# Kernel optimization log

Measured on AMD Instinct MI355X. Metric: run time of the kernel, lower is better.

Reference implementation:

```python
import jax, jax.numpy as jnp
import numpy as np

N_NODES = 50000
N_EDGES = 800000
IN_DIM = 128
HIDDEN = 64
NEG_SLOPE = 0.2


def setup_inputs() -> dict:
    key = jax.random.key(0)
    ks = jax.random.split(key, 8)
    x = jax.random.normal(ks[0], (N_NODES, IN_DIM), dtype=jnp.float32)
    edge_index = jax.random.randint(ks[1], (2, N_EDGES), 0, N_NODES, dtype=jnp.int64)
    # GATConv params (heads=1)
    W = jax.random.normal(ks[2], (HIDDEN, IN_DIM), dtype=jnp.float32) / np.sqrt(IN_DIM)
    att_src = jax.random.normal(ks[3], (HIDDEN,), dtype=jnp.float32) / np.sqrt(HIDDEN)
    att_dst = jax.random.normal(ks[4], (HIDDEN,), dtype=jnp.float32) / np.sqrt(HIDDEN)
    bias_conv = jnp.zeros((HIDDEN,), dtype=jnp.float32)
    # final Linear(hidden, 1)
    W_lin = jax.random.normal(ks[5], (1, HIDDEN), dtype=jnp.float32) / np.sqrt(HIDDEN)
    b_lin = jnp.zeros((1,), dtype=jnp.float32)
    return {"x": x, "edge_index": edge_index, "W": W, "att_src": att_src,
            "att_dst": att_dst, "bias_conv": bias_conv, "W_lin": W_lin, "b_lin": b_lin}


def _gat_forward(x, edge_index, W, att_src, att_dst, bias_conv, W_lin, b_lin):
    n = x.shape[0]
    # add self-loops (PyG GATConv default)
    loop = jnp.arange(n, dtype=edge_index.dtype)
    src = jnp.concatenate([edge_index[0], loop])  # source nodes j (messages from)
    dst = jnp.concatenate([edge_index[1], loop])  # destination nodes i (aggregated at)

    h = x @ W.T                                   # [N, H] projected features
    a_src = h @ att_src                           # [N]
    a_dst = h @ att_dst                           # [N]

    e = jax.nn.leaky_relu(a_src[src] + a_dst[dst], NEG_SLOPE)  # [E']
    # segment softmax over incoming edges of each destination node
    m = jax.ops.segment_max(e, dst, num_segments=n)            # [N]
    ex = jnp.exp(e - m[dst])
    s = jax.ops.segment_sum(ex, dst, num_segments=n)           # [N]
    alpha = ex / s[dst]                                        # [E']

    out = jax.ops.segment_sum(alpha[:, None] * h[src], dst, num_segments=n)
    out = out + bias_conv                         # [N, H]

    out = jax.nn.relu(out)
    # dropout p=0.5 is a no-op in eval mode
    y = jax.nn.sigmoid(out @ W_lin.T + b_lin)     # [N, 1]
    return y


def reference(x, edge_index, W, att_src, att_dst, bias_conv, W_lin, b_lin):
    return _gat_forward(x, edge_index, W, att_src, att_dst, bias_conv, W_lin, b_lin)
```

## Files before the change

### kernel.cpp

```cpp
#include <hip/hip_runtime.h>
#include <hip/hip_bf16.h>
#include <hip/hip_fp16.h>
#include <cstdint>

#define IND 128
#define HID 64
#define NEG_SLOPE 0.2f
#define EPB 4096
#define CBSHIFT 8
#define BCAP 8192
#define SORT_THREADS 256
#define EPT (EPB / SORT_THREADS)
#define QCAP 2048
#define GT 512
#define GSCAN (BCAP / GT)

typedef __attribute__((ext_vector_type(8))) short bf16x8;
typedef __attribute__((ext_vector_type(4))) float f32x4;

__device__ __forceinline__ unsigned short f2bf_bits(float f) {
  __hip_bfloat16 b = __float2bfloat16(f);
  return *reinterpret_cast<unsigned short*>(&b);
}
__device__ __forceinline__ unsigned short f2h_bits(float f) {
  __half h = __float2half(f);
  return *reinterpret_cast<unsigned short*>(&h);
}
__device__ __forceinline__ float h2f_bits(unsigned short u) {
  __half_raw r; r.x = u;
  return __half2float(__half(r));
}
__device__ __forceinline__ float bf2f_bits(unsigned short u) {
  return __uint_as_float((unsigned)u << 16);
}
__device__ __forceinline__ unsigned pack_bf2(float lo, float hi) {
  return (unsigned)f2bf_bits(lo) | ((unsigned)f2bf_bits(hi) << 16);
}
__device__ __forceinline__ bf16x8 mk_bf16x8(unsigned a, unsigned b,
                                            unsigned c, unsigned d) {
  union { unsigned u[4]; bf16x8 v; } t;
  t.u[0] = a; t.u[1] = b; t.u[2] = c; t.u[3] = d;
  return t.v;
}
__device__ __forceinline__ bf16x8 mk_bf16x8_u4(uint4 u) {
  union { uint4 u4; bf16x8 v; } t;
  t.u4 = u;
  return t.v;
}

__global__ __launch_bounds__(256) void k_proj_sort(
    const float* __restrict__ x, const float* __restrict__ W,
    const float* __restrict__ att_s, const float* __restrict__ att_d,
    unsigned short* __restrict__ h, float* __restrict__ a_src,
    float* __restrict__ a_dst,
    const int* __restrict__ ei, int* __restrict__ gcur,
    unsigned* __restrict__ tmp, int E, long long E2,
    int nSort, int nbuck, int n)
{
  __shared__ __align__(16) char smem[20480];
  const int tid = threadIdx.x;

  if (blockIdx.x < (unsigned)nSort) {
    int* hist       = (int*)smem;
    int* sums       = hist + 256;
    int* cur        = sums + 256;
    int* gbase      = cur + 256;
    unsigned* sorted = (unsigned*)(gbase + 256);

    hist[tid] = 0;
    __syncthreads();

    const long long i0 = (long long)blockIdx.x * EPB;

    unsigned pk[EPT];
#pragma unroll
    for (int j = 0; j < EPT; ++j) {
      long long idx = i0 + j * SORT_THREADS + tid;
      unsigned v = 0xFFFFFFFFu;
      if (idx < E2) {
        int s, d;
        if (idx < E) { s = ei[idx]; d = ei[E + idx]; }
        else         { s = d = (int)(idx - E); }
        v = ((unsigned)d << 16) | (unsigned)s;
        atomicAdd(&hist[d >> CBSHIFT], 1);
      }
      pk[j] = v;
    }
    __syncthreads();

    sums[tid] = hist[tid];
    __syncthreads();
    for (int off = 1; off < 256; off <<= 1) {
      int t = (tid >= off) ? sums[tid - off] : 0;
      __syncthreads();
      sums[tid] += t;
      __syncthreads();
    }
    {
      const int lstart_t = sums[tid] - hist[tid];
      cur[tid] = lstart_t;
      gbase[tid] = (tid < nbuck && hist[tid] > 0)
                     ? tid * BCAP + atomicAdd(&gcur[tid], hist[tid]) : 0;
    }
    __syncthreads();
    hist[tid] = sums[tid] - hist[tid];
    __syncthreads();

#pragma unroll
    for (int j = 0; j < EPT; ++j) {
      unsigned v = pk[j];
      if (v != 0xFFFFFFFFu) {
        int b = v >> (16 + CBSHIFT);
        int lpos = atomicAdd(&cur[b], 1);
        sorted[lpos] = v;
      }
    }
    __syncthreads();

    const int cntE = (int)((E2 - i0 < EPB) ? (E2 - i0) : EPB);
    for (int i = tid; i < cntE; i += SORT_THREADS) {
      unsigned v = sorted[i];
      int b = v >> (16 + CBSHIFT);
      tmp[gbase[b] + (i - hist[b])] = v;
    }
    return;
  }

  unsigned* wt = (unsigned*)smem;

  const int nodeBase = (blockIdx.x - nSort) * 64;

#pragma unroll
  for (int it = 0; it < 4; ++it) {
    int fi = (it * 256 + tid) * 8;
    int row = fi >> 7, k = fi & 127;
    float4 w0 = *(const float4*)(W + fi);
    float4 w1 = *(const float4*)(W + fi + 4);
    uint4 pv;
    pv.x = pack_bf2(w0.x, w0.y);
    pv.y = pack_bf2(w0.z, w0.w);
    pv.z = pack_bf2(w1.x, w1.y);
    pv.w = pack_bf2(w1.z, w1.w);
    int c = (k >> 3) ^ ((row >> 2) & 7);
    ((uint4*)wt)[row * 16 + c] = pv;
  }
  __syncthreads();

  const int lane = tid & 63;
  const int wid4 = tid >> 6;
  const int r16  = lane & 15;
  const int q    = lane >> 4;

  const int arow = nodeBase + 16 * wid4 + r16;
  const size_t xoff = (size_t)((arow < n) ? arow : (n - 1)) * IND;

  float4 xv[8];
#pragma unroll
  for (int ks = 0; ks < 4; ++ks) {
    xv[2 * ks]     = *(const float4*)(x + xoff + 32 * ks + 8 * q);
    xv[2 * ks + 1] = *(const float4*)(x + xoff + 32 * ks + 8 * q + 4);
  }

  f32x4 acc0 = {0.f, 0.f, 0.f, 0.f};
  f32x4 acc1 = {0.f, 0.f, 0.f, 0.f};
  f32x4 acc2 = {0.f, 0.f, 0.f, 0.f};
  f32x4 acc3 = {0.f, 0.f, 0.f, 0.f};

#pragma unroll
  for (int ks = 0; ks < 4; ++ks) {
    float4 xa = xv[2 * ks], xb = xv[2 * ks + 1];
    bf16x8 afrag = mk_bf16x8(pack_bf2(xa.x, xa.y), pack_bf2(xa.z, xa.w),
                             pack_bf2(xb.x, xb.y), pack_bf2(xb.z, xb.w));
    {
      int row = r16;
      uint4 bw = ((const uint4*)wt)[row * 16 + ((4 * ks + q) ^ ((row >> 2) & 7))];
      acc0 = __builtin_amdgcn_mfma_f32_16x16x32_bf16(afrag, mk_bf16x8_u4(bw), acc0, 0, 0, 0);
    }
    {
      int row = 16 + r16;
      uint4 bw = ((const uint4*)wt)[row * 16 + ((4 * ks + q) ^ ((row >> 2) & 7))];
      acc1 = __builtin_amdgcn_mfma_f32_16x16x32_bf16(afrag, mk_bf16x8_u4(bw), acc1, 0, 0, 0);
    }
    {
      int row = 32 + r16;
      uint4 bw = ((const uint4*)wt)[row * 16 + ((4 * ks + q) ^ ((row >> 2) & 7))];
      acc2 = __builtin_amdgcn_mfma_f32_16x16x32_bf16(afrag, mk_bf16x8_u4(bw), acc2, 0, 0, 0);
    }
    {
      int row = 48 + r16;
      uint4 bw = ((const uint4*)wt)[row * 16 + ((4 * ks + q) ^ ((row >> 2) & 7))];
      acc3 = __builtin_amdgcn_mfma_f32_16x16x32_bf16(afrag, mk_bf16x8_u4(bw), acc3, 0, 0, 0);
    }
  }

  const float as0 = att_s[r16],      ad0 = att_d[r16];
  const float as1 = att_s[16 + r16], ad1 = att_d[16 + r16];
  const float as2 = att_s[32 + r16], ad2 = att_d[32 + r16];
  const float as3 = att_s[48 + r16], ad3 = att_d[48 + r16];

#pragma unroll
  for (int reg = 0; reg < 4; ++reg) {
    const int node = nodeBase + 16 * wid4 + 4 * q + reg;
    const bool ok = (node < n);
    if (ok) {
      const size_t hb = (size_t)node * HID;
      h[hb + r16]      = f2bf_bits(acc0[reg]);
      h[hb + 16 + r16] = f2bf_bits(acc1[reg]);
      h[hb + 32 + r16] = f2bf_bits(acc2[reg]);
      h[hb + 48 + r16] = f2bf_bits(acc3[reg]);
    }
    float ps = acc0[reg] * as0 + acc1[reg] * as1 + acc2[reg] * as2 + acc3[reg] * as3;
    float pd = acc0[reg] * ad0 + acc1[reg] * ad1 + acc2[reg] * ad2 + acc3[reg] * ad3;
    ps += __shfl_xor(ps, 1, 64); ps += __shfl_xor(ps, 2, 64);
    ps += __shfl_xor(ps, 4, 64); ps += __shfl_xor(ps, 8, 64);
    pd += __shfl_xor(pd, 1, 64); pd += __shfl_xor(pd, 2, 64);
    pd += __shfl_xor(pd, 4, 64); pd += __shfl_xor(pd, 8, 64);
    if (ok && r16 == 0) { a_src[node] = ps; a_dst[node] = pd; }
  }
}

__global__ __launch_bounds__(GT) void k_csr_gather(
    const unsigned* __restrict__ tmp, const int* __restrict__ gcur,
    const float* __restrict__ a_src, const float* __restrict__ a_dst,
    const unsigned short* __restrict__ h,
    const float* __restrict__ bias, const float* __restrict__ W_lin,
    const float* __restrict__ b_lin, float* __restrict__ y, int n)
{
  __shared__ int degl[64], sums[64], cur[64];
  __shared__ float adl[64];
  __shared__ unsigned csrw[QCAP];

  const int tid  = threadIdx.x;
  const int blk  = blockIdx.x;
  const int b    = blk >> 2;
  const int n0   = (b << CBSHIFT) + ((blk & 3) << 6);
  const int base = b * BCAP;
  const int next = base + gcur[b];

  if (tid < 64) {
    degl[tid] = 0;
    const int node = n0 + tid;
    adl[tid] = (node < n) ? a_dst[node] : 0.f;
  }
  __syncthreads();

  unsigned pkv[GSCAN];
#pragma unroll
  for (int j = 0; j < GSCAN; ++j) {
    int i = base + j * GT + tid;
    unsigned v = 0xFFFFFFFFu;
    if (i < next) {
      v = tmp[i];
      unsigned dl = (v >> 16) - (unsigned)n0;
      if (dl < 64u) atomicAdd(&degl[dl], 1);
      else v = 0xFFFFFFFFu;
    }
    pkv[j] = v;
  }
  __syncthreads();

  if (tid < 64) sums[tid] = degl[tid];
  __syncthreads();
  for (int off = 1; off < 64; off <<= 1) {
    int t = (tid >= off && tid < 64) ? sums[tid - off] : 0;
    __syncthreads();
    if (tid < 64) sums[tid] += t;
    __syncthreads();
  }
  if (tid < 64) cur[tid] = sums[tid] - degl[tid];
  __syncthreads();

#pragma unroll
  for (int j = 0; j < GSCAN; ++j) {
    unsigned v = pkv[j];
    if (v != 0xFFFFFFFFu) {
      unsigned dl = (v >> 16) - (unsigned)n0;
      int s = (int)(v & 0xFFFFu);
      float sc = a_src[s] + adl[dl];
      sc = (sc >= 0.f) ? sc : NEG_SLOPE * sc;
      float w = expf(sc);
      int pos = atomicAdd(&cur[dl], 1);
      if (pos < QCAP)
        csrw[pos] = (unsigned)s | ((unsigned)f2h_bits(w) << 16);
    }
  }
  __syncthreads();

  const int lane    = tid & 63;
  const int wid     = tid >> 6;
  const int quarter = lane >> 4;
  const int sub     = lane & 15;

  for (int nl = wid; nl < 64; nl += 8) {
    const int node = n0 + nl;
    if (node >= n) break;

    int rsl = sums[nl] - degl[nl];
    int dg  = degl[nl];
    if (rsl + dg > QCAP) dg = (QCAP > rsl) ? (QCAP - rsl) : 0;
    if (rsl >= QCAP) { rsl = 0; dg = 0; }

    float wpart = 0.f;
    float acc0 = 0.f, acc1 = 0.f, acc2 = 0.f, acc3 = 0.f;

    for (int bb = 0; bb < dg; bb += 64) {
      int i = bb + lane;
      unsigned pk = (i < dg) ? csrw[rsl + i] : 0u;
      wpart += h2f_bits((unsigned short)(pk >> 16));
      const int cnt = (dg - bb < 64) ? (dg - bb) : 64;

      int j = 0;
      for (; j + 8 <= cnt; j += 8) {
#pragma unroll
        for (int g = 0; g < 2; ++g) {
          int e = j + 4 * g + quarter;
          unsigned pe = __shfl(pk, e, 64);
          float we = h2f_bits((unsigned short)(pe >> 16));
          unsigned se = pe & 0xFFFFu;
          ushort4 hb = ((const ushort4*)(h + (size_t)se * HID))[sub];
          acc0 = fmaf(we, bf2f_bits(hb.x), acc0);
          acc1 = fmaf(we, bf2f_bits(hb.y), acc1);
          acc2 = fmaf(we, bf2f_bits(hb.z), acc2);
          acc3 = fmaf(we, bf2f_bits(hb.w), acc3);
        }
      }
      for (; j < cnt; j += 4) {
        int e = j + quarter;
        bool val = e < cnt;
        unsigned pe = __shfl(pk, val ? e : 0, 64);
        float we = val ? h2f_bits((unsigned short)(pe >> 16)) : 0.f;
        unsigned se = val ? (pe & 0xFFFFu) : 0u;
        ushort4 hb = ((const ushort4*)(h + (size_t)se * HID))[sub];
        acc0 = fmaf(we, bf2f_bits(hb.x), acc0);
        acc1 = fmaf(we, bf2f_bits(hb.y), acc1);
        acc2 = fmaf(we, bf2f_bits(hb.z), acc2);
        acc3 = fmaf(we, bf2f_bits(hb.w), acc3);
      }
    }

    acc0 += __shfl_xor(acc0, 16, 64); acc0 += __shfl_xor(acc0, 32, 64);
    acc1 += __shfl_xor(acc1, 16, 64); acc1 += __shfl_xor(acc1, 32, 64);
    acc2 += __shfl_xor(acc2, 16, 64); acc2 += __shfl_xor(acc2, 32, 64);
    acc3 += __shfl_xor(acc3, 16, 64); acc3 += __shfl_xor(acc3, 32, 64);

    float wsum = wpart;
#pragma unroll
    for (int o = 32; o; o >>= 1) wsum += __shfl_xor(wsum, o, 64);
    const float inv = 1.f / wsum;

    float4 bb4 = ((const float4*)bias)[sub];
    float4 ww  = ((const float4*)W_lin)[sub];
    float v0 = fmaxf(acc0 * inv + bb4.x, 0.f);
    float v1 = fmaxf(acc1 * inv + bb4.y, 0.f);
    float v2 = fmaxf(acc2 * inv + bb4.z, 0.f);
    float v3 = fmaxf(acc3 * inv + bb4.w, 0.f);
    float z = v0 * ww.x + v1 * ww.y + v2 * ww.z + v3 * ww.w;
#pragma unroll
    for (int o = 8; o; o >>= 1) z += __shfl_xor(z, o, 64);
    if (lane == 0)
      y[node] = 1.f / (1.f + expf(-(z + b_lin[0])));
  }
}


extern "C" void kernel_launch(void* const* d_in, const int* in_sizes, int n_in,
                              void* d_out, int out_size, void* d_ws, size_t ws_size,
                              hipStream_t stream)
{
  const float* x     = (const float*)d_in[0];
  const int*   ei    = (const int*)d_in[1];
  const float* W     = (const float*)d_in[2];
  const float* att_s = (const float*)d_in[3];
  const float* att_d = (const float*)d_in[4];
  const float* bias  = (const float*)d_in[5];
  const float* W_lin = (const float*)d_in[6];
  const float* b_lin = (const float*)d_in[7];
  float* y = (float*)d_out;

  const int n = in_sizes[0] / IND;
  const int E = in_sizes[1] / 2;
  const long long E2 = (long long)E + n;
  const int nSort = (int)((E2 + EPB - 1) / EPB);
  const int nProj = (n + 63) / 64;
  const int nbuck = (n + (1 << CBSHIFT) - 1) >> CBSHIFT;

  char* ws = (char*)d_ws;
  unsigned short* h = (unsigned short*)ws; ws += (size_t)n * HID * sizeof(unsigned short);
  float*    a_src  = (float*)ws;    ws += (size_t)n * sizeof(float);
  float*    a_dst  = (float*)ws;    ws += (size_t)n * sizeof(float);
  int*      gcur   = (int*)ws;      ws += (size_t)nbuck * sizeof(int);
  unsigned* tmp    = (unsigned*)ws; ws += (size_t)nbuck * BCAP * sizeof(unsigned);

  hipMemsetAsync(gcur, 0, (size_t)nbuck * sizeof(int), stream);

  k_proj_sort<<<nSort + nProj, 256, 0, stream>>>(
      x, W, att_s, att_d, h, a_src, a_dst,
      ei, gcur, tmp, E, E2, nSort, nbuck, n);

  k_csr_gather<<<nbuck * 4, GT, 0, stream>>>(
      tmp, gcur, a_src, a_dst, h, bias, W_lin, b_lin, y, n);
}
```

Measured before the change: 129.9 us.

## Shrink coarse buckets to 64 nodes so each gather block scans only its bucket

```diff
diff --git a/kernel.cpp b/kernel.cpp
--- a/kernel.cpp
+++ b/kernel.cpp
@@ -7,11 +7,11 @@
 #define HID 64
 #define NEG_SLOPE 0.2f
 #define EPB 4096
-#define CBSHIFT 8
-#define BCAP 8192
+#define CBSHIFT 6
+#define BCAP 2048
+#define NBH 784
 #define SORT_THREADS 256
 #define EPT (EPB / SORT_THREADS)
-#define QCAP 2048
 #define GT 512
 #define GSCAN (BCAP / GT)
 
@@ -57,17 +57,18 @@
     unsigned* __restrict__ tmp, int E, long long E2,
     int nSort, int nbuck, int n)
 {
-  __shared__ __align__(16) char smem[20480];
+  __shared__ __align__(16) char smem[29952];
   const int tid = threadIdx.x;
 
   if (blockIdx.x < (unsigned)nSort) {
-    int* hist       = (int*)smem;
-    int* sums       = hist + 256;
-    int* cur        = sums + 256;
-    int* gbase      = cur + 256;
-    unsigned* sorted = (unsigned*)(gbase + 256);
-
-    hist[tid] = 0;
+    int* hist  = (int*)smem;
+    int* locs  = hist + NBH;
+    int* gbase = locs + NBH;
+    int* cur   = gbase + NBH;
+    int* tsum  = cur + NBH;
+    unsigned* sorted = (unsigned*)(tsum + 256);
+
+    for (int i = tid; i < NBH; i += SORT_THREADS) hist[i] = 0;
     __syncthreads();
 
     const long long i0 = (long long)blockIdx.x * EPB;
@@ -88,22 +89,37 @@
     }
     __syncthreads();
 
-    sums[tid] = hist[tid];
+    int t1 = 0, t2 = 0, t3 = 0, tot = 0;
+    const int b0 = tid * 4;
+    if (b0 < NBH) {
+      t1 = hist[b0];
+      t2 = t1 + hist[b0 + 1];
+      t3 = t2 + hist[b0 + 2];
+      tot = t3 + hist[b0 + 3];
+    }
+    tsum[tid] = tot;
     __syncthreads();
     for (int off = 1; off < 256; off <<= 1) {
-      int t = (tid >= off) ? sums[tid - off] : 0;
+      int t = (tid >= off) ? tsum[tid - off] : 0;
       __syncthreads();
-      sums[tid] += t;
+      tsum[tid] += t;
       __syncthreads();
     }
-    {
-      const int lstart_t = sums[tid] - hist[tid];
-      cur[tid] = lstart_t;
-      gbase[tid] = (tid < nbuck && hist[tid] > 0)
-                     ? tid * BCAP + atomicAdd(&gcur[tid], hist[tid]) : 0;
-    }
-    __syncthreads();
-    hist[tid] = sums[tid] - hist[tid];
+    if (b0 < NBH) {
+      const int ex = tsum[tid] - tot;
+      locs[b0]     = ex;
+      locs[b0 + 1] = ex + t1;
+      locs[b0 + 2] = ex + t2;
+      locs[b0 + 3] = ex + t3;
+#pragma unroll
+      for (int k = 0; k < 4; ++k) {
+        const int b = b0 + k;
+        const int c = hist[b];
+        gbase[b] = (b < nbuck && c > 0)
+                     ? b * BCAP + atomicAdd(&gcur[b], c) : 0;
+        cur[b] = locs[b];
+      }
+    }
     __syncthreads();
 
 #pragma unroll
@@ -121,7 +137,8 @@
     for (int i = tid; i < cntE; i += SORT_THREADS) {
       unsigned v = sorted[i];
       int b = v >> (16 + CBSHIFT);
-      tmp[gbase[b] + (i - hist[b])] = v;
+      int slot = gbase[b] + (i - locs[b]);
+      if (slot < (b + 1) * BCAP) tmp[slot] = v;
     }
     return;
   }
@@ -228,14 +245,14 @@
 {
   __shared__ int degl[64], sums[64], cur[64];
   __shared__ float adl[64];
-  __shared__ unsigned csrw[QCAP];
+  __shared__ unsigned csrw[BCAP];
 
   const int tid  = threadIdx.x;
-  const int blk  = blockIdx.x;
-  const int b    = blk >> 2;
-  const int n0   = (b << CBSHIFT) + ((blk & 3) << 6);
+  const int b    = blockIdx.x;
+  const int n0   = b << CBSHIFT;
   const int base = b * BCAP;
-  const int next = base + gcur[b];
+  int run = gcur[b]; if (run > BCAP) run = BCAP;
+  const int next = base + run;
 
   if (tid < 64) {
     degl[tid] = 0;
@@ -280,7 +297,7 @@
       sc = (sc >= 0.f) ? sc : NEG_SLOPE * sc;
       float w = expf(sc);
       int pos = atomicAdd(&cur[dl], 1);
-      if (pos < QCAP)
+      if (pos < BCAP)
         csrw[pos] = (unsigned)s | ((unsigned)f2h_bits(w) << 16);
     }
   }
@@ -297,8 +314,8 @@
 
     int rsl = sums[nl] - degl[nl];
     int dg  = degl[nl];
-    if (rsl + dg > QCAP) dg = (QCAP > rsl) ? (QCAP - rsl) : 0;
-    if (rsl >= QCAP) { rsl = 0; dg = 0; }
+    if (rsl + dg > BCAP) dg = (BCAP > rsl) ? (BCAP - rsl) : 0;
+    if (rsl >= BCAP) { rsl = 0; dg = 0; }
 
     float wpart = 0.f;
     float acc0 = 0.f, acc1 = 0.f, acc2 = 0.f, acc3 = 0.f;
@@ -397,6 +414,6 @@
       x, W, att_s, att_d, h, a_src, a_dst,
       ei, gcur, tmp, E, E2, nSort, nbuck, n);
 
-  k_csr_gather<<<nbuck * 4, GT, 0, stream>>>(
+  k_csr_gather<<<nbuck, GT, 0, stream>>>(
       tmp, gcur, a_src, a_dst, h, bias, W_lin, b_lin, y, n);
 }
```

New measurement: 140.3 us. 8.0% more time.

## Map one node per 16-lane quarter-wave in GAT aggregation instead of per wave

Applied to the files above, without the earlier changes.

```diff
diff --git a/kernel.cpp b/kernel.cpp
--- a/kernel.cpp
+++ b/kernel.cpp
@@ -286,79 +286,56 @@
   }
   __syncthreads();
 
-  const int lane    = tid & 63;
-  const int wid     = tid >> 6;
-  const int quarter = lane >> 4;
-  const int sub     = lane & 15;
-
-  for (int nl = wid; nl < 64; nl += 8) {
+  const int lane = tid & 63;
+  const int wid  = tid >> 6;
+  const int slot = lane >> 4;
+  const int sub  = lane & 15;
+
+  const float4 bb4 = ((const float4*)bias)[sub];
+  const float4 ww  = ((const float4*)W_lin)[sub];
+  const float bl0  = b_lin[0];
+
+#pragma unroll
+  for (int half = 0; half < 2; ++half) {
+    const int nl   = half * 32 + wid * 4 + slot;
     const int node = n0 + nl;
-    if (node >= n) break;
-
-    int rsl = sums[nl] - degl[nl];
-    int dg  = degl[nl];
+    const bool ok  = (node < n);
+
+    int dg  = ok ? degl[nl] : 0;
+    int rsl = ok ? (sums[nl] - dg) : 0;
+    if (rsl >= QCAP) { rsl = 0; dg = 0; }
     if (rsl + dg > QCAP) dg = (QCAP > rsl) ? (QCAP - rsl) : 0;
-    if (rsl >= QCAP) { rsl = 0; dg = 0; }
-
-    float wpart = 0.f;
+
+    int dgm = dg;
+    dgm = max(dgm, __shfl_xor(dgm, 16, 64));
+    dgm = max(dgm, __shfl_xor(dgm, 32, 64));
+
+    float wsum = 0.f;
     float acc0 = 0.f, acc1 = 0.f, acc2 = 0.f, acc3 = 0.f;
 
-    for (int bb = 0; bb < dg; bb += 64) {
-      int i = bb + lane;
-      unsigned pk = (i < dg) ? csrw[rsl + i] : 0u;
-      wpart += h2f_bits((unsigned short)(pk >> 16));
-      const int cnt = (dg - bb < 64) ? (dg - bb) : 64;
-
-      int j = 0;
-      for (; j + 8 <= cnt; j += 8) {
-#pragma unroll
-        for (int g = 0; g < 2; ++g) {
-          int e = j + 4 * g + quarter;
-          unsigned pe = __shfl(pk, e, 64);
-          float we = h2f_bits((unsigned short)(pe >> 16));
-          unsigned se = pe & 0xFFFFu;
-          ushort4 hb = ((const ushort4*)(h + (size_t)se * HID))[sub];
-          acc0 = fmaf(we, bf2f_bits(hb.x), acc0);
-          acc1 = fmaf(we, bf2f_bits(hb.y), acc1);
-          acc2 = fmaf(we, bf2f_bits(hb.z), acc2);
-          acc3 = fmaf(we, bf2f_bits(hb.w), acc3);
-        }
-      }
-      for (; j < cnt; j += 4) {
-        int e = j + quarter;
-        bool val = e < cnt;
-        unsigned pe = __shfl(pk, val ? e : 0, 64);
-        float we = val ? h2f_bits((unsigned short)(pe >> 16)) : 0.f;
-        unsigned se = val ? (pe & 0xFFFFu) : 0u;
-        ushort4 hb = ((const ushort4*)(h + (size_t)se * HID))[sub];
-        acc0 = fmaf(we, bf2f_bits(hb.x), acc0);
-        acc1 = fmaf(we, bf2f_bits(hb.y), acc1);
-        acc2 = fmaf(we, bf2f_bits(hb.z), acc2);
-        acc3 = fmaf(we, bf2f_bits(hb.w), acc3);
-      }
-    }
-
-    acc0 += __shfl_xor(acc0, 16, 64); acc0 += __shfl_xor(acc0, 32, 64);
-    acc1 += __shfl_xor(acc1, 16, 64); acc1 += __shfl_xor(acc1, 32, 64);
-    acc2 += __shfl_xor(acc2, 16, 64); acc2 += __shfl_xor(acc2, 32, 64);
-    acc3 += __shfl_xor(acc3, 16, 64); acc3 += __shfl_xor(acc3, 32, 64);
-
-    float wsum = wpart;
-#pragma unroll
-    for (int o = 32; o; o >>= 1) wsum += __shfl_xor(wsum, o, 64);
+    for (int i = 0; i < dgm; ++i) {
+      const bool v = (i < dg);
+      unsigned pe = csrw[v ? (rsl + i) : 0];
+      float we = v ? h2f_bits((unsigned short)(pe >> 16)) : 0.f;
+      unsigned se = v ? (pe & 0xFFFFu) : 0u;
+      ushort4 hb = ((const ushort4*)(h + (size_t)se * HID))[sub];
+      acc0 = fmaf(we, bf2f_bits(hb.x), acc0);
+      acc1 = fmaf(we, bf2f_bits(hb.y), acc1);
+      acc2 = fmaf(we, bf2f_bits(hb.z), acc2);
+      acc3 = fmaf(we, bf2f_bits(hb.w), acc3);
+      wsum += we;
+    }
+
     const float inv = 1.f / wsum;
-
-    float4 bb4 = ((const float4*)bias)[sub];
-    float4 ww  = ((const float4*)W_lin)[sub];
     float v0 = fmaxf(acc0 * inv + bb4.x, 0.f);
     float v1 = fmaxf(acc1 * inv + bb4.y, 0.f);
     float v2 = fmaxf(acc2 * inv + bb4.z, 0.f);
     float v3 = fmaxf(acc3 * inv + bb4.w, 0.f);
     float z = v0 * ww.x + v1 * ww.y + v2 * ww.z + v3 * ww.w;
-#pragma unroll
-    for (int o = 8; o; o >>= 1) z += __shfl_xor(z, o, 64);
-    if (lane == 0)
-      y[node] = 1.f / (1.f + expf(-(z + b_lin[0])));
+    z += __shfl_xor(z, 1, 64); z += __shfl_xor(z, 2, 64);
+    z += __shfl_xor(z, 4, 64); z += __shfl_xor(z, 8, 64);
+    if (ok && sub == 0)
+      y[node] = 1.f / (1.f + expf(-(z + bl0)));
   }
 }
 
```

Result: faster. 122.7 us (-5.5%).
